# Kernel optimization log

Measured on AMD Instinct MI355X. Metric: run time of the kernel, lower is better.

Reference implementation:

```python
import jax, jax.numpy as jnp
import numpy as np
from jax import lax

B, L, H, E, V = 16, 128, 1024, 512, 32000
MAX_LENGTH = 128
SOS_INDEX = 1
NUM_LAYERS = 2


def setup_inputs() -> dict:
    key = jax.random.key(0)
    ks = jax.random.split(key, 16)
    inp = {}
    inp['input_tensor'] = jax.random.randint(ks[0], (B, L), 0, V)
    inp['target_tensor'] = jax.random.randint(ks[1], (B, L), 0, V)
    inp['true_sample'] = 1
    s = lambda k, shape, fan: jax.random.normal(k, shape, jnp.float32) / np.float32(np.sqrt(fan))
    inp['embedding'] = jax.random.normal(ks[2], (V, E), jnp.float32) * 0.02
    inp['enc_W'] = s(ks[3], (E, H), E)
    inp['enc_b'] = jnp.zeros((H,), jnp.float32)
    inp['Wih0'] = s(ks[4], (E, 3 * H), E)
    inp['Whh0'] = s(ks[5], (H, 3 * H), H)
    inp['bih0'] = jnp.zeros((3 * H,), jnp.float32)
    inp['bhh0'] = jnp.zeros((3 * H,), jnp.float32)
    inp['Wih1'] = s(ks[6], (H, 3 * H), H)
    inp['Whh1'] = s(ks[7], (H, 3 * H), H)
    inp['bih1'] = jnp.zeros((3 * H,), jnp.float32)
    inp['bhh1'] = jnp.zeros((3 * H,), jnp.float32)
    inp['W_out'] = s(ks[8], (2 * H, V), 2 * H)
    inp['b_out'] = jnp.zeros((V,), jnp.float32)
    return inp


def _gru_cell(x, h, Wih, Whh, bih, bhh):
    gx = x @ Wih + bih
    gh = h @ Whh + bhh
    xr, xz, xn = jnp.split(gx, 3, axis=-1)
    hr, hz, hn = jnp.split(gh, 3, axis=-1)
    r = jax.nn.sigmoid(xr + hr)
    z = jax.nn.sigmoid(xz + hz)
    n = jnp.tanh(xn + r * hn)
    return (1.0 - z) * n + z * h


def _forward(input_tensor, true_sample, embedding, enc_W, enc_b,
             Wih0, Whh0, bih0, bhh0, Wih1, Whh1, bih1, bhh1, W_out, b_out):
    batch_size, input_length = input_tensor.shape
    target_length = input_length
    # Encoder: embed + per-timestep projection -> [B, L, H]
    enc_emb = embedding[input_tensor]
    enc_hidden = jnp.tanh(enc_emb @ enc_W + enc_b)
    enc_hidden_t = jnp.transpose(enc_hidden, (1, 0, 2))  # [L, B, H]
    # Pad at the front to max_length (mirrors the copy loop)
    encoder_outputs = jnp.zeros((MAX_LENGTH, batch_size, H), enc_hidden.dtype)
    encoder_outputs = encoder_outputs.at[MAX_LENGTH - input_length:].set(enc_hidden_t)
    # Decoder initial hidden: last encoder state stacked over layers
    h_init = enc_hidden_t[-1]  # [B, H]
    # NOTE: original never updates decoder_input inside the loop -> constant SOS
    x0 = jnp.broadcast_to(embedding[SOS_INDEX], (batch_size, E))
    inv_sqrt_h = np.float32(1.0 / np.sqrt(H))

    def step(carry, _):
        h0, h1 = carry
        h0 = _gru_cell(x0, h0, Wih0, Whh0, bih0, bhh0)
        h1 = _gru_cell(h0, h1, Wih1, Whh1, bih1, bhh1)
        scores = jnp.einsum('bh,lbh->bl', h1, encoder_outputs) * inv_sqrt_h
        attn = jax.nn.softmax(scores, axis=-1)
        ctx = jnp.einsum('bl,lbh->bh', attn, encoder_outputs)
        logits = jnp.concatenate([h1, ctx], axis=-1) @ W_out + b_out
        return (h0, h1), jax.nn.sigmoid(logits)

    _, probs = lax.scan(step, (h_init, h_init), None, length=target_length)
    decoder_outputs = jnp.transpose(probs, (1, 0, 2))  # [B, T, V]
    # Scalar gather: p[b,w] = decoder_outputs[b, w, input_tensor[b, w]]
    out_probabilities = jnp.take_along_axis(decoder_outputs, input_tensor[..., None], axis=2)[..., 0]
    target = jnp.full(input_tensor.shape, np.float32(int(true_sample)), jnp.float32)
    p = jnp.clip(out_probabilities, 1e-12, 1.0 - 1e-7)
    bce = -(target * jnp.log(p) + (1.0 - target) * jnp.log1p(-p))
    loss = jnp.mean(bce) / np.float32(batch_size)
    return loss, out_probabilities


def reference(input_tensor, target_tensor, true_sample, embedding, enc_W, enc_b,
              Wih0, Whh0, bih0, bhh0, Wih1, Whh1, bih1, bhh1, W_out, b_out):
    return _forward(input_tensor, true_sample, embedding, enc_W, enc_b,
                    Wih0, Whh0, bih0, bhh0, Wih1, Whh1, bih1, bhh1, W_out, b_out)
```

## Files before the change

kernel.cpp:

```cpp
#include <hip/hip_runtime.h>
#include <math.h>

#define BB 16
#define LL 128
#define HH 1024
#define EE 512
#define VV 32000
#define G3 3072
#define NBLK 256

__device__ __forceinline__ float sigmoidf_(float x){ return 1.0f/(1.0f+expf(-x)); }

__device__ __forceinline__ float red64(float v){
  v += __shfl_xor(v, 1, 64); v += __shfl_xor(v, 2, 64);
  v += __shfl_xor(v, 4, 64); v += __shfl_xor(v, 8, 64);
  v += __shfl_xor(v, 16, 64); v += __shfl_xor(v, 32, 64);
  return v;
}
__device__ __forceinline__ float red32(float v){
  v += __shfl_xor(v, 1, 64); v += __shfl_xor(v, 2, 64);
  v += __shfl_xor(v, 4, 64); v += __shfl_xor(v, 8, 64);
  v += __shfl_xor(v, 16, 64);
  return v;
}

__global__ void k_rowidx(const int* __restrict__ inp, int* __restrict__ idx){
  int r = blockIdx.x*256 + threadIdx.x;
  if (r < 2048){ int l = r >> 4, b = r & 15; idx[r] = inp[b*LL + l]; }
}

template<int ACT, int KK>
__global__ __launch_bounds__(256) void k_gemm(const float* __restrict__ A, const int* __restrict__ rowidx,
                       const float* __restrict__ Bm, const float* __restrict__ bias,
                       float* __restrict__ C, int N){
  constexpr int KS = (KK==512)?9:10;
  __shared__ float As[32*KK];
  const int tid = threadIdx.x;
  const int r0 = blockIdx.x*32;
  const int c  = blockIdx.y*512 + (tid<<1);
  for (int i = tid; i < 32*KK; i += 256){
    int rr = i >> KS;
    int row = r0 + rr;
    int arow = rowidx ? rowidx[row] : row;
    int kk = i - (rr<<KS);
    As[i] = A[(size_t)arow*KK + kk];
  }
  __syncthreads();
  float2 acc[32];
  #pragma unroll
  for (int r=0;r<32;r++){ acc[r].x=0.f; acc[r].y=0.f; }
  for (int k=0;k<KK;k++){
    const float2 w = *(const float2*)(Bm + (size_t)k*N + c);
    #pragma unroll
    for (int r=0;r<32;r++){
      float a = As[(r<<KS)+k];
      acc[r].x = fmaf(a,w.x,acc[r].x);
      acc[r].y = fmaf(a,w.y,acc[r].y);
    }
  }
  const float2 bv = *(const float2*)(bias + c);
  #pragma unroll
  for (int r=0;r<32;r++){
    float x = acc[r].x + bv.x, y = acc[r].y + bv.y;
    if (ACT==1){ x = tanhf(x); y = tanhf(y); }
    *(float2*)(C + (size_t)(r0+r)*N + c) = make_float2(x,y);
  }
}

__global__ __launch_bounds__(512,1) void k_chains(
    const float* enclast, float* H0all, float* H1all,
    const float* __restrict__ Whh0, const float* __restrict__ Whh1,
    const float* __restrict__ Wih0, const float* __restrict__ Wih1,
    const float* __restrict__ emb,
    const float* __restrict__ bih0, const float* __restrict__ bhh0,
    const float* __restrict__ bhh1, const float* __restrict__ bih1,
    int* flags, int* go)
{
  __shared__ float w0l[12][1024];
  __shared__ float w1l[12][1024];
  __shared__ float wil[12][1024];
  __shared__ float gxbuf[16*12];
  const int tid  = threadIdx.x;
  const int jb   = blockIdx.x << 2;
  const int waveid = tid >> 6;
  const int cgA = waveid >> 2;
  const int bgA = waveid & 3;
  const int kgA = tid & 63;
  const int koffA = kgA << 2;
  const int b0A = bgA << 2;
  const int cgB = waveid >> 1;
  const int bgB = ((waveid & 1) << 1) | ((tid >> 5) & 1);
  const int kgB = tid & 31;
  const int koffB = kgB << 2;
  const int b0B = bgB << 2;
  const int mB  = cgB >> 1;

  const bool pwA = (kgA < 8);
  const int  jlA = (cgA << 1) + (kgA & 1);
  const int  jpA = jb + jlA;
  const int  biA = (kgA >> 1) & 3;
  const int  bA  = b0A + biA;
  const bool pwB = (cgB >= 2) && (kgB < 8);
  const int  jlB = ((cgB & 1) << 1) + (kgB & 1);
  const int  jpB = jb + jlB;
  const int  biB = (kgB >> 1) & 3;
  const int  bB  = b0B + biB;

  float g0r=0.f, g0z=0.f, g0n=0.f;
  {
    for (int idx = tid; idx < 1536; idx += 512){
      int g = idx >> 9, k = idx & 511;
      float4 a = *(const float4*)(Wih0 + (size_t)k*G3 + g*1024 + jb);
      w0l[g*4+0][k]=a.x; w0l[g*4+1][k]=a.y; w0l[g*4+2][k]=a.z; w0l[g*4+3][k]=a.w;
    }
    __syncthreads();
    const float* e1 = emb + EE;
    float ag[6];
    #pragma unroll
    for (int cl=0;cl<6;cl++) ag[cl]=0.f;
    #pragma unroll
    for (int u=0;u<2;u++){
      float4 e = *(const float4*)(e1 + u*256 + koffA);
      #pragma unroll
      for (int cl=0;cl<6;cl++){
        const int gc = ((cl>>1)<<2) + (cgA<<1) + (cl&1);
        const float4 w = *(const float4*)(&w0l[gc][u*256 + koffA]);
        float v = ag[cl];
        v=fmaf(w.x,e.x,v); v=fmaf(w.y,e.y,v); v=fmaf(w.z,e.z,v); v=fmaf(w.w,e.w,v);
        ag[cl]=v;
      }
    }
    #pragma unroll
    for (int cl=0;cl<6;cl++) ag[cl] = red64(ag[cl]);
    if (pwA){
      const int jj = kgA & 1;
      g0r = (jj ? ag[1] : ag[0]) + bih0[jpA];
      g0z = (jj ? ag[3] : ag[2]) + bih0[1024+jpA];
      g0n = (jj ? ag[5] : ag[4]) + bih0[2048+jpA];
    }
    __syncthreads();
  }

  for (int idx = tid; idx < 3072; idx += 512){
    int g = idx >> 10, k = idx & 1023;
    float4 a = *(const float4*)(Whh0 + (size_t)k*G3 + g*1024 + jb);
    w0l[g*4+0][k]=a.x; w0l[g*4+1][k]=a.y; w0l[g*4+2][k]=a.z; w0l[g*4+3][k]=a.w;
    float4 d = *(const float4*)(Whh1 + (size_t)k*G3 + g*1024 + jb);
    w1l[g*4+0][k]=d.x; w1l[g*4+1][k]=d.y; w1l[g*4+2][k]=d.z; w1l[g*4+3][k]=d.w;
    float4 e = *(const float4*)(Wih1 + (size_t)k*G3 + g*1024 + jb);
    wil[g*4+0][k]=e.x; wil[g*4+1][k]=e.y; wil[g*4+2][k]=e.z; wil[g*4+3][k]=e.w;
  }
  float b0rA=0.f,b0zA=0.f,b0nA=0.f;
  if (pwA){ b0rA = bhh0[jpA]; b0zA = bhh0[1024+jpA]; b0nA = bhh0[2048+jpA]; }
  float birB=0.f,bizB=0.f,binB=0.f,b1rB=0.f,b1zB=0.f,b1nB=0.f;
  if (pwB){
    birB = bih1[jpB]; bizB = bih1[1024+jpB]; binB = bih1[2048+jpB];
    b1rB = bhh1[jpB]; b1zB = bhh1[1024+jpB]; b1nB = bhh1[2048+jpB];
  }
  __syncthreads();

  const int myflag = (int)blockIdx.x * 32;

  for (int t = 0; t <= LL; ++t){
    if (t >= 1){
      if (blockIdx.x == 0){
        if (tid < 256){
          while (__hip_atomic_load(&flags[tid*32], __ATOMIC_RELAXED,
                                   __HIP_MEMORY_SCOPE_AGENT) < t)
            __builtin_amdgcn_s_sleep(1);
        }
        __syncthreads();
        if (tid == 0)
          __hip_atomic_store(go, t, __ATOMIC_RELAXED, __HIP_MEMORY_SCOPE_AGENT);
      } else {
        if (tid == 0){
          while (__hip_atomic_load(go, __ATOMIC_RELAXED,
                                   __HIP_MEMORY_SCOPE_AGENT) < t)
            __builtin_amdgcn_s_sleep(1);
        }
        __syncthreads();
      }
    }

    if (t >= 1){
      const float* hp0 = H0all + (size_t)(t-1)*(BB*HH);
      const float* hp1 = (t==1) ? enclast : (H1all + (size_t)(t-2)*(BB*HH));
      const float* hr  = mB ? hp1 : hp0;
      float hprev1 = 0.f;
      if (pwB) hprev1 = hp1[(size_t)bB*HH + jpB];

      float accB[6][4];
      #pragma unroll
      for (int cl=0;cl<6;cl++)
        #pragma unroll
        for (int bi=0;bi<4;bi++) accB[cl][bi]=0.f;

      #pragma unroll
      for (int u=0;u<8;u++){
        float4 h4[4];
        #pragma unroll
        for (int bi=0;bi<4;bi++)
          h4[bi] = *(const float4*)(hr + (size_t)(b0B+bi)*HH + u*128 + koffB);
        #pragma unroll
        for (int cl=0;cl<6;cl++){
          const int gc = ((cl>>1)<<2) + ((cgB&1)<<1) + (cl&1);
          const float4 w = mB ? *(const float4*)(&w1l[gc][u*128 + koffB])
                              : *(const float4*)(&wil[gc][u*128 + koffB]);
          #pragma unroll
          for (int bi=0;bi<4;bi++){
            float v = accB[cl][bi];
            v=fmaf(w.x,h4[bi].x,v); v=fmaf(w.y,h4[bi].y,v);
            v=fmaf(w.z,h4[bi].z,v); v=fmaf(w.w,h4[bi].w,v);
            accB[cl][bi]=v;
          }
        }
      }
      #pragma unroll
      for (int cl=0;cl<6;cl++)
        #pragma unroll
        for (int bi=0;bi<4;bi++) accB[cl][bi] = red32(accB[cl][bi]);

      if (mB == 0){
        #pragma unroll
        for (int cl=0;cl<6;cl++){
          if (kgB == cl){
            const int g = cl >> 1;
            const int jl = ((cgB&1)<<1) + (cl&1);
            #pragma unroll
            for (int bi=0;bi<4;bi++)
              gxbuf[(b0B+bi)*12 + g*4 + jl] = accB[cl][bi];
          }
        }
      }
      __syncthreads();
      if (pwB){
        float ghr=0.f, ghz=0.f, ghn=0.f;
        #pragma unroll
        for (int jj=0;jj<2;jj++)
          #pragma unroll
          for (int ii=0;ii<4;ii++){
            bool sel = ((kgB&1)==jj) & (biB==ii);
            ghr = sel ? accB[jj][ii]   : ghr;
            ghz = sel ? accB[2+jj][ii] : ghz;
            ghn = sel ? accB[4+jj][ii] : ghn;
          }
        float gxr = gxbuf[bB*12 + 0*4 + jlB];
        float gxz = gxbuf[bB*12 + 1*4 + jlB];
        float gxn = gxbuf[bB*12 + 2*4 + jlB];
        float r = sigmoidf_(gxr + birB + ghr + b1rB);
        float z = sigmoidf_(gxz + bizB + ghz + b1zB);
        float n = tanhf    (gxn + binB + r*(ghn + b1nB));
        float hnew = (1.f-z)*n + z*hprev1;
        __hip_atomic_store((int*)&H1all[(size_t)(t-1)*(BB*HH) + (size_t)bB*HH + jpB],
                           __float_as_int(hnew),
                           __ATOMIC_RELAXED, __HIP_MEMORY_SCOPE_AGENT);
      }
    }

    if (t < LL){
      const float* hp0 = (t==0) ? enclast : (H0all + (size_t)(t-1)*(BB*HH));
      float hprev0 = 0.f;
      if (pwA) hprev0 = hp0[(size_t)bA*HH + jpA];

      float acc0[6][4];
      #pragma unroll
      for (int cl=0;cl<6;cl++)
        #pragma unroll
        for (int bi=0;bi<4;bi++) acc0[cl][bi]=0.f;

      #pragma unroll
      for (int u=0;u<4;u++){
        float4 h4[4];
        #pragma unroll
        for (int bi=0;bi<4;bi++)
          h4[bi] = *(const float4*)(hp0 + (size_t)(b0A+bi)*HH + u*256 + koffA);
        #pragma unroll
        for (int cl=0;cl<6;cl++){
          const int gc = ((cl>>1)<<2) + (cgA<<1) + (cl&1);
          const float4 w = *(const float4*)(&w0l[gc][u*256 + koffA]);
          #pragma unroll
          for (int bi=0;bi<4;bi++){
            float v = acc0[cl][bi];
            v=fmaf(w.x,h4[bi].x,v); v=fmaf(w.y,h4[bi].y,v);
            v=fmaf(w.z,h4[bi].z,v); v=fmaf(w.w,h4[bi].w,v);
            acc0[cl][bi]=v;
          }
        }
      }
      #pragma unroll
      for (int cl=0;cl<6;cl++)
        #pragma unroll
        for (int bi=0;bi<4;bi++) acc0[cl][bi] = red64(acc0[cl][bi]);

      if (pwA){
        float ghr=0.f, ghz=0.f, ghn=0.f;
        #pragma unroll
        for (int jj=0;jj<2;jj++)
          #pragma unroll
          for (int ii=0;ii<4;ii++){
            bool sel = ((kgA&1)==jj) & (biA==ii);
            ghr = sel ? acc0[jj][ii]   : ghr;
            ghz = sel ? acc0[2+jj][ii] : ghz;
            ghn = sel ? acc0[4+jj][ii] : ghn;
          }
        float r = sigmoidf_(g0r + ghr + b0rA);
        float z = sigmoidf_(g0z + ghz + b0zA);
        float n = tanhf    (g0n + r*(ghn + b0nA));
        float hnew = (1.f-z)*n + z*hprev0;
        __hip_atomic_store((int*)&H0all[(size_t)t*(BB*HH) + (size_t)bA*HH + jpA],
                           __float_as_int(hnew),
                           __ATOMIC_RELAXED, __HIP_MEMORY_SCOPE_AGENT);
      }
    }

    if (t < LL){
      asm volatile("s_waitcnt vmcnt(0)" ::: "memory");
      __syncthreads();
      if (tid == 0)
        __hip_atomic_store(&flags[myflag], t+1,
                           __ATOMIC_RELAXED, __HIP_MEMORY_SCOPE_AGENT);
    }
  }
}

__global__ __launch_bounds__(256) void k_attn(const float* __restrict__ enc, const float* __restrict__ H1,
                       float* __restrict__ ctx){
  __shared__ float h1s[8][HH];
  __shared__ float sc[8][LL];
  __shared__ float part[2][8][LL];
  const int tid = threadIdx.x;
  const int s0 = blockIdx.x*8, b = blockIdx.y;
  for (int i = tid; i < 8*HH; i += 256){
    int si = i >> 10, k = i & 1023;
    h1s[si][k] = H1[(size_t)(s0+si)*BB*HH + (size_t)b*HH + k];
  }
  __syncthreads();
  {
    const int l = tid & 127, half = tid >> 7;
    const float4* er = (const float4*)(enc + ((size_t)l*BB + b)*HH + half*512);
    float a[8];
    #pragma unroll
    for (int s=0;s<8;s++) a[s]=0.f;
    for (int q=0;q<128;q++){
      float4 e = er[q];
      #pragma unroll
      for (int s=0;s<8;s++){
        const float4 h = *(const float4*)(&h1s[s][half*512 + q*4]);
        a[s] += h.x*e.x + h.y*e.y + h.z*e.z + h.w*e.w;
      }
    }
    #pragma unroll
    for (int s=0;s<8;s++) part[half][s][l] = a[s];
  }
  __syncthreads();
  for (int p = tid; p < 1024; p += 256){
    int s = p >> 7, l = p & 127;
    sc[s][l] = (part[0][s][l] + part[1][s][l]) * 0.03125f;
  }
  __syncthreads();
  {
    int s = tid >> 5, lid = tid & 31;
    float v0 = sc[s][lid], v1 = sc[s][lid+32], v2 = sc[s][lid+64], v3 = sc[s][lid+96];
    float m = fmaxf(fmaxf(v0,v1),fmaxf(v2,v3));
    for (int off=16; off>=1; off>>=1) m = fmaxf(m, __shfl_xor(m, off, 32));
    float e0=__expf(v0-m), e1=__expf(v1-m), e2=__expf(v2-m), e3=__expf(v3-m);
    float ssum = e0+e1+e2+e3;
    for (int off=16; off>=1; off>>=1) ssum += __shfl_xor(ssum, off, 32);
    float inv = 1.0f/ssum;
    sc[s][lid]=e0*inv; sc[s][lid+32]=e1*inv; sc[s][lid+64]=e2*inv; sc[s][lid+96]=e3*inv;
  }
  __syncthreads();
  {
    float acc[4][8];
    #pragma unroll
    for (int q=0;q<4;q++)
      #pragma unroll
      for (int s=0;s<8;s++) acc[q][s]=0.f;
    for (int l=0;l<128;l++){
      const float* er = enc + ((size_t)l*BB + b)*HH + tid;
      float a[8];
      #pragma unroll
      for (int s=0;s<8;s++) a[s] = sc[s][l];
      #pragma unroll
      for (int q=0;q<4;q++){
        float e = er[q*256];
        #pragma unroll
        for (int s=0;s<8;s++) acc[q][s] = fmaf(a[s], e, acc[q][s]);
      }
    }
    #pragma unroll
    for (int s=0;s<8;s++)
      #pragma unroll
      for (int q=0;q<4;q++)
        ctx[(size_t)(s0+s)*BB*HH + (size_t)b*HH + tid + q*256] = acc[q][s];
  }
}

__global__ __launch_bounds__(256) void k_logit(const float* __restrict__ H1, const float* __restrict__ ctx,
                        const float* __restrict__ Wout, const float* __restrict__ bout,
                        const int* __restrict__ inp, const int* __restrict__ ts,
                        float* __restrict__ outp, float* __restrict__ bce){
  __shared__ float rbuf[256];
  const int i = blockIdx.x;
  const int b = i >> 7, t = i & 127;
  const int v = inp[b*LL + t];
  const int tid = threadIdx.x;
  const float* h1r = H1 + ((size_t)t*BB + b)*HH;
  const float* cxr = ctx + ((size_t)t*BB + b)*HH;
  float acc = 0.f;
  #pragma unroll
  for (int q=0;q<4;q++){
    int k = tid + q*256;
    acc = fmaf(h1r[k], Wout[(size_t)k*VV + v], acc);
  }
  #pragma unroll
  for (int q=0;q<4;q++){
    int k = tid + q*256;
    acc = fmaf(cxr[k], Wout[(size_t)(k+1024)*VV + v], acc);
  }
  rbuf[tid] = acc;
  __syncthreads();
  for (int s=128; s>0; s>>=1){
    if (tid < s) rbuf[tid] += rbuf[tid+s];
    __syncthreads();
  }
  if (tid==0){
    float logit = rbuf[0] + bout[v];
    float p = 1.0f/(1.0f + expf(-logit));
    outp[b*LL + t] = p;
    float pc = fminf(fmaxf(p, 1e-12f), 1.0f - 1e-7f);
    float tg = (float)ts[0];
    bce[i] = -(tg*logf(pc) + (1.0f-tg)*log1pf(-pc));
  }
}

__global__ void k_loss(const float* __restrict__ bce, float* __restrict__ out0){
  __shared__ float rbuf[256];
  int tid = threadIdx.x;
  float s = 0.f;
  for (int i = tid; i < 2048; i += 256) s += bce[i];
  rbuf[tid] = s; __syncthreads();
  for (int st=128; st>0; st>>=1){
    if (tid<st) rbuf[tid]+=rbuf[tid+st];
    __syncthreads();
  }
  if (tid==0) out0[0] = rbuf[0] * (1.0f/(2048.0f*16.0f));
}

extern "C" void kernel_launch(void* const* d_in, const int* in_sizes, int n_in,
                              void* d_out, int out_size, void* d_ws, size_t ws_size,
                              hipStream_t stream){
  (void)in_sizes; (void)n_in; (void)out_size; (void)ws_size;
  const int*   inp   = (const int*)d_in[0];
  const int*   ts    = (const int*)d_in[2];
  const float* emb   = (const float*)d_in[3];
  const float* encW  = (const float*)d_in[4];
  const float* encb  = (const float*)d_in[5];
  const float* Wih0  = (const float*)d_in[6];
  const float* Whh0  = (const float*)d_in[7];
  const float* bih0  = (const float*)d_in[8];
  const float* bhh0  = (const float*)d_in[9];
  const float* Wih1  = (const float*)d_in[10];
  const float* Whh1  = (const float*)d_in[11];
  const float* bih1  = (const float*)d_in[12];
  const float* bhh1  = (const float*)d_in[13];
  const float* Wout  = (const float*)d_in[14];
  const float* bout  = (const float*)d_in[15];
  float* out = (float*)d_out;

  float* ws      = (float*)d_ws;
  float* enc_out = ws;
  float* H0      = enc_out + 2097152;
  float* H1      = H0 + 2097152;
  float* GX1     = H1 + 2097152;
  float* CTX     = GX1 + 6291456;
  float* gx0     = CTX + 2097152;
  float* bceb    = gx0 + 3072;
  int*   rowidx  = (int*)(bceb + 2048);
  int*   flags   = rowidx + 2048;
  int*   go      = flags + 256*32;

  hipMemsetAsync(flags, 0, (256*32 + 32)*sizeof(int), stream);
  k_rowidx<<<8,256,0,stream>>>(inp, rowidx);
  k_gemm<1,512><<<dim3(64,2),256,0,stream>>>(emb, rowidx, encW, encb, enc_out, HH);

  const float* enclast = enc_out + (size_t)127*BB*HH;

  k_chains<<<NBLK,512,0,stream>>>(enclast, H0, H1, Whh0, Whh1, Wih0, Wih1, emb,
                                  bih0, bhh0, bhh1, bih1, flags, go);
  k_attn<<<dim3(16,16),256,0,stream>>>(enc_out, H1, CTX);
  k_logit<<<2048,256,0,stream>>>(H1, CTX, Wout, bout, inp, ts, out+1, bceb);
  k_loss<<<1,256,0,stream>>>(bceb, out);
}
```

Before: 2.070 ms.

## Skew layer-1 GRU one extra step and precompute its input gates before barrier

Restructures the persistent recurrent kernel so layer 1 lags layer 0 by two steps instead of one. The layer-1 input projection (Wih1·h0) is now computed before the grid-wide barrier wait, overlapping it with synchronization latency. The layer-1 hidden projection then runs after layer 0 using the full block with 64-lane reductions, replacing the split-wave scheme and its shared gx buffer. This adds one extra loop iteration and more serial work per step after the barrier, in exchange for hiding part of the layer-1 work behind the barrier.

```diff
diff --git a/kernel.cpp b/kernel.cpp
--- a/kernel.cpp
+++ b/kernel.cpp
@@ -15,12 +15,6 @@
   v += __shfl_xor(v, 1, 64); v += __shfl_xor(v, 2, 64);
   v += __shfl_xor(v, 4, 64); v += __shfl_xor(v, 8, 64);
   v += __shfl_xor(v, 16, 64); v += __shfl_xor(v, 32, 64);
-  return v;
-}
-__device__ __forceinline__ float red32(float v){
-  v += __shfl_xor(v, 1, 64); v += __shfl_xor(v, 2, 64);
-  v += __shfl_xor(v, 4, 64); v += __shfl_xor(v, 8, 64);
-  v += __shfl_xor(v, 16, 64);
   return v;
 }
 
@@ -79,7 +73,6 @@
   __shared__ float w0l[12][1024];
   __shared__ float w1l[12][1024];
   __shared__ float wil[12][1024];
-  __shared__ float gxbuf[16*12];
   const int tid  = threadIdx.x;
   const int jb   = blockIdx.x << 2;
   const int waveid = tid >> 6;
@@ -88,23 +81,11 @@
   const int kgA = tid & 63;
   const int koffA = kgA << 2;
   const int b0A = bgA << 2;
-  const int cgB = waveid >> 1;
-  const int bgB = ((waveid & 1) << 1) | ((tid >> 5) & 1);
-  const int kgB = tid & 31;
-  const int koffB = kgB << 2;
-  const int b0B = bgB << 2;
-  const int mB  = cgB >> 1;
-
   const bool pwA = (kgA < 8);
-  const int  jlA = (cgA << 1) + (kgA & 1);
-  const int  jpA = jb + jlA;
-  const int  biA = (kgA >> 1) & 3;
-  const int  bA  = b0A + biA;
-  const bool pwB = (cgB >= 2) && (kgB < 8);
-  const int  jlB = ((cgB & 1) << 1) + (kgB & 1);
-  const int  jpB = jb + jlB;
-  const int  biB = (kgB >> 1) & 3;
-  const int  bB  = b0B + biB;
+  const int jlA = (cgA << 1) + (kgA & 1);
+  const int jpA = jb + jlA;
+  const int biA = (kgA >> 1) & 3;
+  const int bA  = b0A + biA;
 
   float g0r=0.f, g0z=0.f, g0n=0.f;
   {
@@ -151,17 +132,49 @@
     wil[g*4+0][k]=e.x; wil[g*4+1][k]=e.y; wil[g*4+2][k]=e.z; wil[g*4+3][k]=e.w;
   }
   float b0rA=0.f,b0zA=0.f,b0nA=0.f;
-  if (pwA){ b0rA = bhh0[jpA]; b0zA = bhh0[1024+jpA]; b0nA = bhh0[2048+jpA]; }
-  float birB=0.f,bizB=0.f,binB=0.f,b1rB=0.f,b1zB=0.f,b1nB=0.f;
-  if (pwB){
-    birB = bih1[jpB]; bizB = bih1[1024+jpB]; binB = bih1[2048+jpB];
-    b1rB = bhh1[jpB]; b1zB = bhh1[1024+jpB]; b1nB = bhh1[2048+jpB];
+  float birA=0.f,bizA=0.f,binA=0.f,b1rA=0.f,b1zA=0.f,b1nA=0.f;
+  if (pwA){
+    b0rA = bhh0[jpA]; b0zA = bhh0[1024+jpA]; b0nA = bhh0[2048+jpA];
+    birA = bih1[jpA]; bizA = bih1[1024+jpA]; binA = bih1[2048+jpA];
+    b1rA = bhh1[jpA]; b1zA = bhh1[1024+jpA]; b1nA = bhh1[2048+jpA];
   }
   __syncthreads();
 
   const int myflag = (int)blockIdx.x * 32;
 
-  for (int t = 0; t <= LL; ++t){
+  for (int t = 0; t <= LL+1; ++t){
+    float accg[6][4];
+    if (t >= 2){
+      const float* hg = H0all + (size_t)(t-2)*(BB*HH);
+      #pragma unroll
+      for (int cl=0;cl<6;cl++)
+        #pragma unroll
+        for (int bi=0;bi<4;bi++) accg[cl][bi]=0.f;
+      #pragma unroll
+      for (int u=0;u<4;u++){
+        float4 h4[4];
+        #pragma unroll
+        for (int bi=0;bi<4;bi++)
+          h4[bi] = *(const float4*)(hg + (size_t)(b0A+bi)*HH + u*256 + koffA);
+        #pragma unroll
+        for (int cl=0;cl<6;cl++){
+          const int gc = ((cl>>1)<<2) + (cgA<<1) + (cl&1);
+          const float4 w = *(const float4*)(&wil[gc][u*256 + koffA]);
+          #pragma unroll
+          for (int bi=0;bi<4;bi++){
+            float v = accg[cl][bi];
+            v=fmaf(w.x,h4[bi].x,v); v=fmaf(w.y,h4[bi].y,v);
+            v=fmaf(w.z,h4[bi].z,v); v=fmaf(w.w,h4[bi].w,v);
+            accg[cl][bi]=v;
+          }
+        }
+      }
+      #pragma unroll
+      for (int cl=0;cl<6;cl++)
+        #pragma unroll
+        for (int bi=0;bi<4;bi++) accg[cl][bi] = red64(accg[cl][bi]);
+    }
+
     if (t >= 1){
       if (blockIdx.x == 0){
         if (tid < 256){
@@ -182,81 +195,6 @@
       }
     }
 
-    if (t >= 1){
-      const float* hp0 = H0all + (size_t)(t-1)*(BB*HH);
-      const float* hp1 = (t==1) ? enclast : (H1all + (size_t)(t-2)*(BB*HH));
-      const float* hr  = mB ? hp1 : hp0;
-      float hprev1 = 0.f;
-      if (pwB) hprev1 = hp1[(size_t)bB*HH + jpB];
-
-      float accB[6][4];
-      #pragma unroll
-      for (int cl=0;cl<6;cl++)
-        #pragma unroll
-        for (int bi=0;bi<4;bi++) accB[cl][bi]=0.f;
-
-      #pragma unroll
-      for (int u=0;u<8;u++){
-        float4 h4[4];
-        #pragma unroll
-        for (int bi=0;bi<4;bi++)
-          h4[bi] = *(const float4*)(hr + (size_t)(b0B+bi)*HH + u*128 + koffB);
-        #pragma unroll
-        for (int cl=0;cl<6;cl++){
-          const int gc = ((cl>>1)<<2) + ((cgB&1)<<1) + (cl&1);
-          const float4 w = mB ? *(const float4*)(&w1l[gc][u*128 + koffB])
-                              : *(const float4*)(&wil[gc][u*128 + koffB]);
-          #pragma unroll
-          for (int bi=0;bi<4;bi++){
-            float v = accB[cl][bi];
-            v=fmaf(w.x,h4[bi].x,v); v=fmaf(w.y,h4[bi].y,v);
-            v=fmaf(w.z,h4[bi].z,v); v=fmaf(w.w,h4[bi].w,v);
-            accB[cl][bi]=v;
-          }
-        }
-      }
-      #pragma unroll
-      for (int cl=0;cl<6;cl++)
-        #pragma unroll
-        for (int bi=0;bi<4;bi++) accB[cl][bi] = red32(accB[cl][bi]);
-
-      if (mB == 0){
-        #pragma unroll
-        for (int cl=0;cl<6;cl++){
-          if (kgB == cl){
-            const int g = cl >> 1;
-            const int jl = ((cgB&1)<<1) + (cl&1);
-            #pragma unroll
-            for (int bi=0;bi<4;bi++)
-              gxbuf[(b0B+bi)*12 + g*4 + jl] = accB[cl][bi];
-          }
-        }
-      }
-      __syncthreads();
-      if (pwB){
-        float ghr=0.f, ghz=0.f, ghn=0.f;
-        #pragma unroll
-        for (int jj=0;jj<2;jj++)
-          #pragma unroll
-          for (int ii=0;ii<4;ii++){
-            bool sel = ((kgB&1)==jj) & (biB==ii);
-            ghr = sel ? accB[jj][ii]   : ghr;
-            ghz = sel ? accB[2+jj][ii] : ghz;
-            ghn = sel ? accB[4+jj][ii] : ghn;
-          }
-        float gxr = gxbuf[bB*12 + 0*4 + jlB];
-        float gxz = gxbuf[bB*12 + 1*4 + jlB];
-        float gxn = gxbuf[bB*12 + 2*4 + jlB];
-        float r = sigmoidf_(gxr + birB + ghr + b1rB);
-        float z = sigmoidf_(gxz + bizB + ghz + b1zB);
-        float n = tanhf    (gxn + binB + r*(ghn + b1nB));
-        float hnew = (1.f-z)*n + z*hprev1;
-        __hip_atomic_store((int*)&H1all[(size_t)(t-1)*(BB*HH) + (size_t)bB*HH + jpB],
-                           __float_as_int(hnew),
-                           __ATOMIC_RELAXED, __HIP_MEMORY_SCOPE_AGENT);
-      }
-    }
-
     if (t < LL){
       const float* hp0 = (t==0) ? enclast : (H0all + (size_t)(t-1)*(BB*HH));
       float hprev0 = 0.f;
@@ -267,7 +205,6 @@
       for (int cl=0;cl<6;cl++)
         #pragma unroll
         for (int bi=0;bi<4;bi++) acc0[cl][bi]=0.f;
-
       #pragma unroll
       for (int u=0;u<4;u++){
         float4 h4[4];
@@ -313,13 +250,69 @@
       }
     }
 
-    if (t < LL){
-      asm volatile("s_waitcnt vmcnt(0)" ::: "memory");
-      __syncthreads();
-      if (tid == 0)
-        __hip_atomic_store(&flags[myflag], t+1,
+    if (t >= 2){
+      const float* hp1 = (t==2) ? enclast : (H1all + (size_t)(t-3)*(BB*HH));
+      float hprev1 = 0.f;
+      if (pwA) hprev1 = hp1[(size_t)bA*HH + jpA];
+
+      float acc1[6][4];
+      #pragma unroll
+      for (int cl=0;cl<6;cl++)
+        #pragma unroll
+        for (int bi=0;bi<4;bi++) acc1[cl][bi]=0.f;
+      #pragma unroll
+      for (int u=0;u<4;u++){
+        float4 h4[4];
+        #pragma unroll
+        for (int bi=0;bi<4;bi++)
+          h4[bi] = *(const float4*)(hp1 + (size_t)(b0A+bi)*HH + u*256 + koffA);
+        #pragma unroll
+        for (int cl=0;cl<6;cl++){
+          const int gc = ((cl>>1)<<2) + (cgA<<1) + (cl&1);
+          const float4 w = *(const float4*)(&w1l[gc][u*256 + koffA]);
+          #pragma unroll
+          for (int bi=0;bi<4;bi++){
+            float v = acc1[cl][bi];
+            v=fmaf(w.x,h4[bi].x,v); v=fmaf(w.y,h4[bi].y,v);
+            v=fmaf(w.z,h4[bi].z,v); v=fmaf(w.w,h4[bi].w,v);
+            acc1[cl][bi]=v;
+          }
+        }
+      }
+      #pragma unroll
+      for (int cl=0;cl<6;cl++)
+        #pragma unroll
+        for (int bi=0;bi<4;bi++) acc1[cl][bi] = red64(acc1[cl][bi]);
+
+      if (pwA){
+        float ghr=0.f, ghz=0.f, ghn=0.f, gxr=0.f, gxz=0.f, gxn=0.f;
+        #pragma unroll
+        for (int jj=0;jj<2;jj++)
+          #pragma unroll
+          for (int ii=0;ii<4;ii++){
+            bool sel = ((kgA&1)==jj) & (biA==ii);
+            ghr = sel ? acc1[jj][ii]   : ghr;
+            ghz = sel ? acc1[2+jj][ii] : ghz;
+            ghn = sel ? acc1[4+jj][ii] : ghn;
+            gxr = sel ? accg[jj][ii]   : gxr;
+            gxz = sel ? accg[2+jj][ii] : gxz;
+            gxn = sel ? accg[4+jj][ii] : gxn;
+          }
+        float r = sigmoidf_(gxr + birA + ghr + b1rA);
+        float z = sigmoidf_(gxz + bizA + ghz + b1zA);
+        float n = tanhf    (gxn + binA + r*(ghn + b1nA));
+        float hnew = (1.f-z)*n + z*hprev1;
+        __hip_atomic_store((int*)&H1all[(size_t)(t-2)*(BB*HH) + (size_t)bA*HH + jpA],
+                           __float_as_int(hnew),
                            __ATOMIC_RELAXED, __HIP_MEMORY_SCOPE_AGENT);
-    }
+      }
+    }
+
+    asm volatile("s_waitcnt vmcnt(0)" ::: "memory");
+    __syncthreads();
+    if (tid == 0)
+      __hip_atomic_store(&flags[myflag], t+1,
+                         __ATOMIC_RELAXED, __HIP_MEMORY_SCOPE_AGENT);
   }
 }
 
@@ -480,7 +473,7 @@
   int*   flags   = rowidx + 2048;
   int*   go      = flags + 256*32;
 
-  hipMemsetAsync(flags, 0, (256*32 + 32)*sizeof(int), stream);
+  (void)hipMemsetAsync(flags, 0, (256*32 + 32)*sizeof(int), stream);
   k_rowidx<<<8,256,0,stream>>>(inp, rowidx);
   k_gemm<1,512><<<dim3(64,2),256,0,stream>>>(emb, rowidx, encW, encb, enc_out, HH);
 
```

New measurement: 2.113 ms. 2.1% more time.
